# Optimization experiments

Measured on AMD Instinct MI355X. Metric: run time of the kernel, lower is better.

## Reference

```python
import jax, jax.numpy as jnp
import numpy as np

B, F, D = 16384, 32, 64
EPS = 1e-5


def layer_norm(x, g, b):
    m = x.mean(-1, keepdims=True)
    v = ((x - m) ** 2).mean(-1, keepdims=True)
    return (x - m) / jnp.sqrt(v + EPS) * g + b


def setup_inputs() -> dict:
    key = jax.random.key(0)
    ks = jax.random.split(key, 24)
    IN = F * D

    def w(k, shape, fan_in):
        return jax.random.normal(k, shape, dtype=jnp.float32) / np.sqrt(fan_in)

    return {
        "x": jax.random.normal(ks[0], (B, F, D), dtype=jnp.float32),
        # StaticGRN (mask branch): Linear(IN,D) -> ELU -> Linear(D,F); skip Linear(IN,F); GateAndNorm(F)
        "mw1": w(ks[1], (IN, D), IN), "mb1": jnp.zeros((D,), jnp.float32),
        "mw2": w(ks[2], (D, F), D), "mb2": jnp.zeros((F,), jnp.float32),
        "mlw": w(ks[3], (IN, F), IN), "mlb": jnp.zeros((F,), jnp.float32),
        "mgw": w(ks[4], (F, F), F), "mgb": jnp.zeros((F,), jnp.float32),
        "mlw2": w(ks[5], (F, F), F), "mlb2": jnp.zeros((F,), jnp.float32),
        "mgamma": jnp.ones((F,), jnp.float32), "mbeta": jnp.zeros((F,), jnp.float32),
        # Per-feature GRNNoContext params, stacked over F (batched small GEMMs)
        "w1": w(ks[6], (F, D, D), D), "b1": jnp.zeros((F, D), jnp.float32),
        "w2": w(ks[7], (F, D, D), D), "b2": jnp.zeros((F, D), jnp.float32),
        "gw": w(ks[8], (F, D, D), D), "gb": jnp.zeros((F, D), jnp.float32),
        "lw": w(ks[9], (F, D, D), D), "lb": jnp.zeros((F, D), jnp.float32),
        "gamma": jnp.ones((F, D), jnp.float32), "beta": jnp.zeros((F, D), jnp.float32),
    }


def reference(x, mw1, mb1, mw2, mb2, mlw, mlb, mgw, mgb, mlw2, mlb2, mgamma, mbeta,
              w1, b1, w2, b2, gw, gb, lw, lb, gamma, beta):
    b, f, d = x.shape
    flat = x.reshape(b, f * d)
    # StaticGRN mask branch (dropout is 0.0 -> identity)
    h = jax.nn.elu(flat @ mw1 + mb1) @ mw2 + mb2          # [B,F]
    res = flat @ mlw + mlb                                 # [B,F] skip path
    pre = jax.nn.sigmoid(h @ mgw + mgb) * (h @ mlw2 + mlb2) + res
    mask = jax.nn.softmax(layer_norm(pre, mgamma, mbeta), axis=-1)[:, None, :]  # [B,1,F]
    # Per-feature GRNs, batched over the feature axis
    hh = jax.nn.elu(jnp.einsum('bfd,fde->bfe', x, w1) + b1)
    hh = jnp.einsum('bfd,fde->bfe', hh, w2) + b2
    gate = jax.nn.sigmoid(jnp.einsum('bfd,fde->bfe', hh, gw) + gb)
    lin = jnp.einsum('bfd,fde->bfe', hh, lw) + lb
    vecs = layer_norm(gate * lin + x, gamma, beta)         # [B,F,D]
    out = jnp.einsum('bof,bfd->bod', mask, vecs)[:, 0, :]  # [B,D]
    return out, mask
```

## Files before the change

### kernel.cpp

```cpp
#include <hip/hip_runtime.h>
#include <hip/hip_bf16.h>
#include <math.h>

#define NB 16384
#define NF 32
#define ND 64
#define NIN 2048

typedef __attribute__((ext_vector_type(8))) short fragA;
typedef __attribute__((ext_vector_type(4))) float fragC;

#define MFMA(a, b, c) __builtin_amdgcn_mfma_f32_16x16x32_bf16((a), (b), (c), 0, 0, 0)

__device__ __forceinline__ short f2bf(float f) {
    union { float f; unsigned u; } v; v.f = f;
    return (short)((v.u + 0x7fffu + ((v.u >> 16) & 1u)) >> 16);
}
__device__ __forceinline__ fragA cvt8(const float* p) {
    const float4 a = *(const float4*)p;
    const float4 b = *(const float4*)(p + 4);
    union { __hip_bfloat162 h[4]; fragA f; } u;
    u.h[0] = __float22bfloat162_rn(make_float2(a.x, a.y));
    u.h[1] = __float22bfloat162_rn(make_float2(a.z, a.w));
    u.h[2] = __float22bfloat162_rn(make_float2(b.x, b.y));
    u.h[3] = __float22bfloat162_rn(make_float2(b.z, b.w));
    return u.f;
}

__global__ __launch_bounds__(256) void prep_kernel(
    const float* __restrict__ w1, const float* __restrict__ w2,
    const float* __restrict__ gw, const float* __restrict__ lw,
    const float* __restrict__ mw1, const float* __restrict__ mlw,
    const float* __restrict__ mw2, const float* __restrict__ mgw,
    const float* __restrict__ mlw2,
    short* __restrict__ wsout)
{
    int F = blockIdx.x * 256 + threadIdx.x;
    fragA o;
    if (F < 65536) {
        int mat = F >> 14;
        int f   = (F >> 9) & 31;
        int nt  = (F >> 7) & 3;
        int s   = (F >> 6) & 1;
        int l   = F & 63;
        const float* src = (mat == 0 ? w1 : mat == 1 ? w2 : mat == 2 ? gw : lw)
                           + (size_t)f * 4096;
        int n  = nt * 16 + (l & 15);
        int k0 = s * 32 + ((l >> 4) << 3);
#pragma unroll
        for (int j = 0; j < 8; ++j) o[j] = f2bf(src[(k0 + j) * 64 + n]);
    } else if (F < 90112) {
        int G  = F - 65536;
        int f  = G / 768;
        int r  = G - f * 768;
        int nt = r >> 7;
        int s  = (r >> 6) & 1;
        int l  = r & 63;
        int n  = nt * 16 + (l & 15);
        int k0 = f * 64 + s * 32 + ((l >> 4) << 3);
        if (n < 64) {
#pragma unroll
            for (int j = 0; j < 8; ++j) o[j] = f2bf(mw1[(size_t)(k0 + j) * 64 + n]);
        } else {
#pragma unroll
            for (int j = 0; j < 8; ++j) o[j] = f2bf(mlw[(size_t)(k0 + j) * 32 + (n - 64)]);
        }
    } else {
        int G2 = F - 90112;
        if (G2 < 256) {
            int nt = G2 >> 7, s = (G2 >> 6) & 1, l = G2 & 63;
            int n = nt * 16 + (l & 15);
            int k0 = s * 32 + ((l >> 4) << 3);
#pragma unroll
            for (int j = 0; j < 8; ++j) o[j] = f2bf(mw2[(k0 + j) * 32 + n]);
        } else {
            int G3 = G2 - 256;
            const float* src = (G3 < 128) ? mgw : mlw2;
            G3 &= 127;
            int nt = G3 >> 6, l = G3 & 63;
            int n = nt * 16 + (l & 15);
            int k0 = (l >> 4) << 3;
#pragma unroll
            for (int j = 0; j < 8; ++j) o[j] = f2bf(src[(k0 + j) * 32 + n]);
        }
    }
    ((fragA*)wsout)[F] = o;
}

__global__ __launch_bounds__(256, 4) void fused_kernel(
    const float* __restrict__ x,
    const short* __restrict__ wfrag, const short* __restrict__ mwfrag,
    const short* __restrict__ swfrag,
    const float* __restrict__ mb1, const float* __restrict__ mb2,
    const float* __restrict__ mlb, const float* __restrict__ mgb,
    const float* __restrict__ mlb2,
    const float* __restrict__ mgamma, const float* __restrict__ mbeta,
    const float* __restrict__ b1, const float* __restrict__ b2,
    const float* __restrict__ gb, const float* __restrict__ lb,
    const float* __restrict__ gamma, const float* __restrict__ beta,
    float* __restrict__ mask_out, float* __restrict__ out)
{
    __shared__ float smem[8960];
    float* redS  = smem;
    float* gS    = smem;
    float* lS    = smem + 768;
    float* hS1   = smem + 1552;
    float* resS  = smem + 2640;
    float* h2S   = smem + 3216;
    float* outS  = smem + 4352;
    float* maskS = smem + 8448;

    const int tid = threadIdx.x;
    const int w = tid >> 6, l = tid & 63;
    const int row0 = blockIdx.x * 16;
    const int m = l & 15, q = l >> 4;

    const fragA* wf  = (const fragA*)wfrag;
    const fragA* mwf = (const fragA*)mwfrag;
    const fragA* swf = (const fragA*)swfrag;

    for (int i = tid; i < 1552; i += 256) redS[i] = 0.f;
    __syncthreads();

    fragC acc[6];
#pragma unroll
    for (int nt = 0; nt < 6; ++nt) acc[nt] = (fragC){0.f, 0.f, 0.f, 0.f};

    const float* xpm = x + (size_t)(row0 + m) * NIN + q * 8;
    for (int fi = 0; fi < 8; ++fi) {
        int f = w * 8 + fi;
        const float* xp = xpm + f * ND;
        fragA a0 = cvt8(xp), a1 = cvt8(xp + 32);
        const size_t fb = (size_t)f * 768 + l;
#pragma unroll
        for (int nt = 0; nt < 6; ++nt) {
            acc[nt] = MFMA(a0, mwf[fb + nt * 128], acc[nt]);
            acc[nt] = MFMA(a1, mwf[fb + nt * 128 + 64], acc[nt]);
        }
    }
#pragma unroll
    for (int nt = 0; nt < 6; ++nt)
#pragma unroll
        for (int rg = 0; rg < 4; ++rg)
            atomicAdd(&redS[(q * 4 + rg) * 97 + nt * 16 + m], acc[nt][rg]);
    __syncthreads();

    {
        int r = tid & 15, cb = tid >> 4;
#pragma unroll
        for (int i = 0; i < 6; ++i) {
            int c = cb + i * 16;
            float s = redS[r * 97 + c];
            if (c < 64) {
                float v = s + mb1[c];
                hS1[r * 68 + c] = v > 0.f ? v : expm1f(v);
            } else {
                resS[r * 36 + (c - 64)] = s + mlb[c - 64];
            }
        }
    }
    __syncthreads();

    if (w < 2) {
        const float* ap = hS1 + m * 68 + q * 8;
        fragA a0 = cvt8(ap), a1 = cvt8(ap + 32);
        fragC c = {0.f, 0.f, 0.f, 0.f};
        c = MFMA(a0, swf[w * 128 + l], c);
        c = MFMA(a1, swf[w * 128 + 64 + l], c);
        float bv = mb2[w * 16 + m];
#pragma unroll
        for (int rg = 0; rg < 4; ++rg)
            h2S[(q * 4 + rg) * 36 + w * 16 + m] = c[rg] + bv;
    }
    __syncthreads();

    {
        int ntc = w & 1;
        int isl = w >> 1;
        fragA a = cvt8(h2S + m * 36 + q * 8);
        fragC c = {0.f, 0.f, 0.f, 0.f};
        c = MFMA(a, swf[256 + isl * 128 + ntc * 64 + l], c);
        float* dst = isl ? lS : gS;
#pragma unroll
        for (int rg = 0; rg < 4; ++rg)
            dst[(q * 4 + rg) * 36 + ntc * 16 + m] = c[rg];
    }
    __syncthreads();

    if (w == 0) {
        int r2 = l >> 2, c0 = (l & 3) * 8;
        float pre[8];
#pragma unroll
        for (int i = 0; i < 8; ++i) {
            int c = c0 + i;
            float gg = gS[r2 * 36 + c] + mgb[c];
            float ll = lS[r2 * 36 + c] + mlb2[c];
            pre[i] = ll / (1.f + expf(-gg)) + resS[r2 * 36 + c];
        }
        float s1 = 0.f;
#pragma unroll
        for (int i = 0; i < 8; ++i) s1 += pre[i];
        s1 += __shfl_xor(s1, 1); s1 += __shfl_xor(s1, 2);
        float mean = s1 * (1.f / 32.f);
        float s2 = 0.f;
#pragma unroll
        for (int i = 0; i < 8; ++i) { float d = pre[i] - mean; s2 += d * d; }
        s2 += __shfl_xor(s2, 1); s2 += __shfl_xor(s2, 2);
        float inv = rsqrtf(s2 * (1.f / 32.f) + 1e-5f);
        float ln[8]; float mx = -3.4e38f;
#pragma unroll
        for (int i = 0; i < 8; ++i) {
            ln[i] = (pre[i] - mean) * inv * mgamma[c0 + i] + mbeta[c0 + i];
            mx = fmaxf(mx, ln[i]);
        }
        mx = fmaxf(mx, __shfl_xor(mx, 1));
        mx = fmaxf(mx, __shfl_xor(mx, 2));
        float ssum = 0.f;
#pragma unroll
        for (int i = 0; i < 8; ++i) { ln[i] = expf(ln[i] - mx); ssum += ln[i]; }
        ssum += __shfl_xor(ssum, 1); ssum += __shfl_xor(ssum, 2);
        float rs = 1.f / ssum;
        float* mo = mask_out + (size_t)(row0 + r2) * 32 + c0;
        *(float4*)mo       = (float4){ln[0] * rs, ln[1] * rs, ln[2] * rs, ln[3] * rs};
        *(float4*)(mo + 4) = (float4){ln[4] * rs, ln[5] * rs, ln[6] * rs, ln[7] * rs};
#pragma unroll
        for (int i = 0; i < 8; ++i) maskS[r2 * 32 + c0 + i] = ln[i] * rs;
    }
    __syncthreads();

    float* hW = smem + w * 1088;

    fragC oac[4];
#pragma unroll
    for (int nt = 0; nt < 4; ++nt) oac[nt] = (fragC){0.f, 0.f, 0.f, 0.f};

    for (int fi = 0; fi < 8; ++fi) {
        int f = w * 8 + fi;
        float xres[4][4];
#pragma unroll
        for (int rg = 0; rg < 4; ++rg)
#pragma unroll
            for (int nt = 0; nt < 4; ++nt)
                xres[rg][nt] = x[(size_t)(row0 + q * 4 + rg) * NIN + f * ND + nt * 16 + m];
        float b1v[4], b2v[4], gbv[4], lbv[4], gmv[4], btv[4];
#pragma unroll
        for (int nt = 0; nt < 4; ++nt) {
            int c = f * 64 + nt * 16 + m;
            b1v[nt] = b1[c]; b2v[nt] = b2[c]; gbv[nt] = gb[c];
            lbv[nt] = lb[c]; gmv[nt] = gamma[c]; btv[nt] = beta[c];
        }
        float mk[4];
#pragma unroll
        for (int rg = 0; rg < 4; ++rg) mk[rg] = maskS[(q * 4 + rg) * 32 + f];

        {
            const float* xp = xpm + f * ND;
            fragA a0 = cvt8(xp), a1 = cvt8(xp + 32);
            const size_t base = (size_t)f * 512 + l;
#pragma unroll
            for (int nt = 0; nt < 4; ++nt) {
                fragC c = {0.f, 0.f, 0.f, 0.f};
                c = MFMA(a0, wf[base + nt * 128], c);
                c = MFMA(a1, wf[base + nt * 128 + 64], c);
                int col = nt * 16 + m;
#pragma unroll
                for (int rg = 0; rg < 4; ++rg) {
                    float v = c[rg] + b1v[nt];
                    hW[(q * 4 + rg) * 68 + col] = v > 0.f ? v : expm1f(v);
                }
            }
        }
        {
            const float* ap = hW + m * 68 + q * 8;
            fragA a0 = cvt8(ap), a1 = cvt8(ap + 32);
            const size_t base = ((size_t)(NF + f)) * 512 + l;
            fragC cc[4];
#pragma unroll
            for (int nt = 0; nt < 4; ++nt) {
                fragC c = {0.f, 0.f, 0.f, 0.f};
                c = MFMA(a0, wf[base + nt * 128], c);
                c = MFMA(a1, wf[base + nt * 128 + 64], c);
                cc[nt] = c;
            }
#pragma unroll
            for (int nt = 0; nt < 4; ++nt) {
                int col = nt * 16 + m;
#pragma unroll
                for (int rg = 0; rg < 4; ++rg)
                    hW[(q * 4 + rg) * 68 + col] = cc[nt][rg] + b2v[nt];
            }
        }
        {
            const float* ap = hW + m * 68 + q * 8;
            fragA a0 = cvt8(ap), a1 = cvt8(ap + 32);
            const size_t baseg = ((size_t)(2 * NF + f)) * 512 + l;
            const size_t basel = ((size_t)(3 * NF + f)) * 512 + l;
            fragC ga[4], la[4];
#pragma unroll
            for (int nt = 0; nt < 4; ++nt) {
                fragC g = {0.f, 0.f, 0.f, 0.f}, li = {0.f, 0.f, 0.f, 0.f};
                g  = MFMA(a0, wf[baseg + nt * 128], g);
                g  = MFMA(a1, wf[baseg + nt * 128 + 64], g);
                li = MFMA(a0, wf[basel + nt * 128], li);
                li = MFMA(a1, wf[basel + nt * 128 + 64], li);
                ga[nt] = g; la[nt] = li;
            }
#pragma unroll
            for (int rg = 0; rg < 4; ++rg) {
                float val[4];
#pragma unroll
                for (int nt = 0; nt < 4; ++nt) {
                    float gg = ga[nt][rg] + gbv[nt];
                    float ll = la[nt][rg] + lbv[nt];
                    val[nt] = ll / (1.f + expf(-gg)) + xres[rg][nt];
                }
                float s1 = val[0] + val[1] + val[2] + val[3];
                s1 += __shfl_xor(s1, 1); s1 += __shfl_xor(s1, 2);
                s1 += __shfl_xor(s1, 4); s1 += __shfl_xor(s1, 8);
                float mean = s1 * (1.f / 64.f);
                float s2 = 0.f;
#pragma unroll
                for (int nt = 0; nt < 4; ++nt) { float d = val[nt] - mean; s2 += d * d; }
                s2 += __shfl_xor(s2, 1); s2 += __shfl_xor(s2, 2);
                s2 += __shfl_xor(s2, 4); s2 += __shfl_xor(s2, 8);
                float inv = rsqrtf(s2 * (1.f / 64.f) + 1e-5f);
#pragma unroll
                for (int nt = 0; nt < 4; ++nt) {
                    float vec = (val[nt] - mean) * inv * gmv[nt] + btv[nt];
                    oac[nt][rg] += mk[rg] * vec;
                }
            }
        }
    }

#pragma unroll
    for (int nt = 0; nt < 4; ++nt)
#pragma unroll
        for (int rg = 0; rg < 4; ++rg)
            outS[w * 1024 + (q * 4 + rg) * 64 + nt * 16 + m] = oac[nt][rg];
    __syncthreads();
    {
        int t4 = tid * 4;
        int r = t4 >> 6, c = t4 & 63;
        float v[4];
#pragma unroll
        for (int j = 0; j < 4; ++j) {
            v[j] = outS[r * 64 + c + j] + outS[1024 + r * 64 + c + j]
                 + outS[2048 + r * 64 + c + j] + outS[3072 + r * 64 + c + j];
        }
        *(float4*)(out + (size_t)(row0 + r) * 64 + c) = (float4){v[0], v[1], v[2], v[3]};
    }
}

extern "C" void kernel_launch(void* const* d_in, const int* in_sizes, int n_in,
                              void* d_out, int out_size, void* d_ws, size_t ws_size,
                              hipStream_t stream) {
    const float* x      = (const float*)d_in[0];
    const float* mw1    = (const float*)d_in[1];
    const float* mb1    = (const float*)d_in[2];
    const float* mw2    = (const float*)d_in[3];
    const float* mb2    = (const float*)d_in[4];
    const float* mlw    = (const float*)d_in[5];
    const float* mlb    = (const float*)d_in[6];
    const float* mgw    = (const float*)d_in[7];
    const float* mgb    = (const float*)d_in[8];
    const float* mlw2   = (const float*)d_in[9];
    const float* mlb2   = (const float*)d_in[10];
    const float* mgamma = (const float*)d_in[11];
    const float* mbeta  = (const float*)d_in[12];
    const float* w1     = (const float*)d_in[13];
    const float* b1     = (const float*)d_in[14];
    const float* w2     = (const float*)d_in[15];
    const float* b2     = (const float*)d_in[16];
    const float* gw     = (const float*)d_in[17];
    const float* gb     = (const float*)d_in[18];
    const float* lw     = (const float*)d_in[19];
    const float* lb     = (const float*)d_in[20];
    const float* gamma  = (const float*)d_in[21];
    const float* beta   = (const float*)d_in[22];

    float* out  = (float*)d_out;
    float* mask = out + (size_t)NB * 64;

    short* wfrag  = (short*)d_ws;
    short* mwfrag = wfrag + (size_t)65536 * 8;
    short* swfrag = wfrag + (size_t)90112 * 8;

    hipLaunchKernelGGL(prep_kernel, dim3(354), dim3(256), 0, stream,
                       w1, w2, gw, lw, mw1, mlw, mw2, mgw, mlw2, wfrag);
    hipLaunchKernelGGL(fused_kernel, dim3(NB / 16), dim3(256), 0, stream,
                       x, wfrag, mwfrag, swfrag,
                       mb1, mb2, mlb, mgb, mlb2, mgamma, mbeta,
                       b1, b2, gb, lb, gamma, beta,
                       mask, out);
}
```

Measured before the change: 347.5 us.

## Replace LDS atomics with per-wave partials, fast-math epilogues, reorder per-feature GRN loads

The first-stage cross-wave reduction now has each wave write its partial tile to its own LDS slot, and one pass sums the four slots. This removes the zero-init pass, a barrier and the LDS atomics. ELU, sigmoid and softmax use __expf and hardware reciprocal, and layer norm computes sum and sum of squares in a single shuffle pass. The per-feature loop prefetches w2 fragments into registers and moves the residual, bias and mask loads to later points so their latency overlaps with MFMA work. Risks are lower accuracy from the fast intrinsics and the one-pass variance, plus higher register pressure from the prefetched fragments.

```diff
diff --git a/kernel.cpp b/kernel.cpp
--- a/kernel.cpp
+++ b/kernel.cpp
@@ -26,6 +26,10 @@
     u.h[3] = __float22bfloat162_rn(make_float2(b.z, b.w));
     return u.f;
 }
+
+__device__ __forceinline__ float frcp(float x) { return __builtin_amdgcn_rcpf(x); }
+__device__ __forceinline__ float felu(float v) { return v > 0.f ? v : __expf(v) - 1.f; }
+__device__ __forceinline__ float fsig(float g) { return __builtin_amdgcn_rcpf(1.f + __expf(-g)); }
 
 __global__ __launch_bounds__(256) void prep_kernel(
     const float* __restrict__ w1, const float* __restrict__ w2,
@@ -104,9 +108,9 @@
     float* redS  = smem;
     float* gS    = smem;
     float* lS    = smem + 768;
-    float* hS1   = smem + 1552;
-    float* resS  = smem + 2640;
-    float* h2S   = smem + 3216;
+    float* hS1   = smem + 6208;
+    float* resS  = smem + 7296;
+    float* h2S   = smem + 7872;
     float* outS  = smem + 4352;
     float* maskS = smem + 8448;
 
@@ -118,9 +122,6 @@
     const fragA* wf  = (const fragA*)wfrag;
     const fragA* mwf = (const fragA*)mwfrag;
     const fragA* swf = (const fragA*)swfrag;
-
-    for (int i = tid; i < 1552; i += 256) redS[i] = 0.f;
-    __syncthreads();
 
     fragC acc[6];
 #pragma unroll
@@ -138,11 +139,14 @@
             acc[nt] = MFMA(a1, mwf[fb + nt * 128 + 64], acc[nt]);
         }
     }
-#pragma unroll
-    for (int nt = 0; nt < 6; ++nt)
-#pragma unroll
-        for (int rg = 0; rg < 4; ++rg)
-            atomicAdd(&redS[(q * 4 + rg) * 97 + nt * 16 + m], acc[nt][rg]);
+    {
+        float* myred = redS + w * 1552;
+#pragma unroll
+        for (int nt = 0; nt < 6; ++nt)
+#pragma unroll
+            for (int rg = 0; rg < 4; ++rg)
+                myred[(q * 4 + rg) * 97 + nt * 16 + m] = acc[nt][rg];
+    }
     __syncthreads();
 
     {
@@ -150,10 +154,10 @@
 #pragma unroll
         for (int i = 0; i < 6; ++i) {
             int c = cb + i * 16;
-            float s = redS[r * 97 + c];
+            float s = redS[r * 97 + c]        + redS[1552 + r * 97 + c]
+                    + redS[3104 + r * 97 + c] + redS[4656 + r * 97 + c];
             if (c < 64) {
-                float v = s + mb1[c];
-                hS1[r * 68 + c] = v > 0.f ? v : expm1f(v);
+                hS1[r * 68 + c] = felu(s + mb1[c]);
             } else {
                 resS[r * 36 + (c - 64)] = s + mlb[c - 64];
             }
@@ -195,18 +199,16 @@
             int c = c0 + i;
             float gg = gS[r2 * 36 + c] + mgb[c];
             float ll = lS[r2 * 36 + c] + mlb2[c];
-            pre[i] = ll / (1.f + expf(-gg)) + resS[r2 * 36 + c];
-        }
-        float s1 = 0.f;
-#pragma unroll
-        for (int i = 0; i < 8; ++i) s1 += pre[i];
-        s1 += __shfl_xor(s1, 1); s1 += __shfl_xor(s1, 2);
+            pre[i] = ll * fsig(gg) + resS[r2 * 36 + c];
+        }
+        float s1 = 0.f, s2 = 0.f;
+#pragma unroll
+        for (int i = 0; i < 8; ++i) { s1 += pre[i]; s2 += pre[i] * pre[i]; }
+        s1 += __shfl_xor(s1, 1); s2 += __shfl_xor(s2, 1);
+        s1 += __shfl_xor(s1, 2); s2 += __shfl_xor(s2, 2);
         float mean = s1 * (1.f / 32.f);
-        float s2 = 0.f;
-#pragma unroll
-        for (int i = 0; i < 8; ++i) { float d = pre[i] - mean; s2 += d * d; }
-        s2 += __shfl_xor(s2, 1); s2 += __shfl_xor(s2, 2);
-        float inv = rsqrtf(s2 * (1.f / 32.f) + 1e-5f);
+        float var  = s2 * (1.f / 32.f) - mean * mean;
+        float inv  = rsqrtf(fmaxf(var, 0.f) + 1e-5f);
         float ln[8]; float mx = -3.4e38f;
 #pragma unroll
         for (int i = 0; i < 8; ++i) {
@@ -217,9 +219,9 @@
         mx = fmaxf(mx, __shfl_xor(mx, 2));
         float ssum = 0.f;
 #pragma unroll
-        for (int i = 0; i < 8; ++i) { ln[i] = expf(ln[i] - mx); ssum += ln[i]; }
+        for (int i = 0; i < 8; ++i) { ln[i] = __expf(ln[i] - mx); ssum += ln[i]; }
         ssum += __shfl_xor(ssum, 1); ssum += __shfl_xor(ssum, 2);
-        float rs = 1.f / ssum;
+        float rs = frcp(ssum);
         float* mo = mask_out + (size_t)(row0 + r2) * 32 + c0;
         *(float4*)mo       = (float4){ln[0] * rs, ln[1] * rs, ln[2] * rs, ln[3] * rs};
         *(float4*)(mo + 4) = (float4){ln[4] * rs, ln[5] * rs, ln[6] * rs, ln[7] * rs};
@@ -235,100 +237,105 @@
     for (int nt = 0; nt < 4; ++nt) oac[nt] = (fragC){0.f, 0.f, 0.f, 0.f};
 
     for (int fi = 0; fi < 8; ++fi) {
-        int f = w * 8 + fi;
+        const int f = w * 8 + fi;
+        const size_t base1 = (size_t)f * 512 + l;
+        const size_t base2 = (size_t)(NF + f) * 512 + l;
+        const size_t baseg = (size_t)(2 * NF + f) * 512 + l;
+        const size_t basel = (size_t)(3 * NF + f) * 512 + l;
+
+        const float* xp = xpm + f * ND;
+        fragA a0 = cvt8(xp), a1 = cvt8(xp + 32);
+        fragC c1[4];
+#pragma unroll
+        for (int nt = 0; nt < 4; ++nt) {
+            fragC c = {0.f, 0.f, 0.f, 0.f};
+            c = MFMA(a0, wf[base1 + nt * 128], c);
+            c = MFMA(a1, wf[base1 + nt * 128 + 64], c);
+            c1[nt] = c;
+        }
+        fragA w2f[8];
+#pragma unroll
+        for (int j = 0; j < 4; ++j) {
+            w2f[j]     = wf[base2 + j * 128];
+            w2f[j + 4] = wf[base2 + j * 128 + 64];
+        }
+#pragma unroll
+        for (int nt = 0; nt < 4; ++nt) {
+            float bv = b1[f * 64 + nt * 16 + m];
+            int col = nt * 16 + m;
+#pragma unroll
+            for (int rg = 0; rg < 4; ++rg)
+                hW[(q * 4 + rg) * 68 + col] = felu(c1[nt][rg] + bv);
+        }
+        const float* ap = hW + m * 68 + q * 8;
+        fragA h0 = cvt8(ap), h1 = cvt8(ap + 32);
+        fragC c2[4];
+#pragma unroll
+        for (int nt = 0; nt < 4; ++nt) {
+            fragC c = {0.f, 0.f, 0.f, 0.f};
+            c = MFMA(h0, w2f[nt], c);
+            c = MFMA(h1, w2f[nt + 4], c);
+            c2[nt] = c;
+        }
         float xres[4][4];
 #pragma unroll
         for (int rg = 0; rg < 4; ++rg)
 #pragma unroll
             for (int nt = 0; nt < 4; ++nt)
                 xres[rg][nt] = x[(size_t)(row0 + q * 4 + rg) * NIN + f * ND + nt * 16 + m];
-        float b1v[4], b2v[4], gbv[4], lbv[4], gmv[4], btv[4];
-#pragma unroll
-        for (int nt = 0; nt < 4; ++nt) {
-            int c = f * 64 + nt * 16 + m;
-            b1v[nt] = b1[c]; b2v[nt] = b2[c]; gbv[nt] = gb[c];
-            lbv[nt] = lb[c]; gmv[nt] = gamma[c]; btv[nt] = beta[c];
-        }
         float mk[4];
 #pragma unroll
         for (int rg = 0; rg < 4; ++rg) mk[rg] = maskS[(q * 4 + rg) * 32 + f];
-
-        {
-            const float* xp = xpm + f * ND;
-            fragA a0 = cvt8(xp), a1 = cvt8(xp + 32);
-            const size_t base = (size_t)f * 512 + l;
+#pragma unroll
+        for (int nt = 0; nt < 4; ++nt) {
+            float bv = b2[f * 64 + nt * 16 + m];
+            int col = nt * 16 + m;
+#pragma unroll
+            for (int rg = 0; rg < 4; ++rg)
+                hW[(q * 4 + rg) * 68 + col] = c2[nt][rg] + bv;
+        }
+        const float* ap2 = hW + m * 68 + q * 8;
+        fragA g0 = cvt8(ap2), g1 = cvt8(ap2 + 32);
+        fragC ga[4], la[4];
+#pragma unroll
+        for (int nt = 0; nt < 4; ++nt) {
+            fragC g = {0.f, 0.f, 0.f, 0.f}, li = {0.f, 0.f, 0.f, 0.f};
+            g  = MFMA(g0, wf[baseg + nt * 128], g);
+            g  = MFMA(g1, wf[baseg + nt * 128 + 64], g);
+            li = MFMA(g0, wf[basel + nt * 128], li);
+            li = MFMA(g1, wf[basel + nt * 128 + 64], li);
+            ga[nt] = g; la[nt] = li;
+        }
+        float gbv[4], lbv[4], gmv[4], btv[4];
+#pragma unroll
+        for (int nt = 0; nt < 4; ++nt) {
+            int cidx = f * 64 + nt * 16 + m;
+            gbv[nt] = gb[cidx]; lbv[nt] = lb[cidx];
+            gmv[nt] = gamma[cidx]; btv[nt] = beta[cidx];
+        }
+#pragma unroll
+        for (int rg = 0; rg < 4; ++rg) {
+            float val[4];
 #pragma unroll
             for (int nt = 0; nt < 4; ++nt) {
-                fragC c = {0.f, 0.f, 0.f, 0.f};
-                c = MFMA(a0, wf[base + nt * 128], c);
-                c = MFMA(a1, wf[base + nt * 128 + 64], c);
-                int col = nt * 16 + m;
-#pragma unroll
-                for (int rg = 0; rg < 4; ++rg) {
-                    float v = c[rg] + b1v[nt];
-                    hW[(q * 4 + rg) * 68 + col] = v > 0.f ? v : expm1f(v);
-                }
+                float gg = ga[nt][rg] + gbv[nt];
+                float ll = la[nt][rg] + lbv[nt];
+                val[nt] = ll * fsig(gg) + xres[rg][nt];
             }
-        }
-        {
-            const float* ap = hW + m * 68 + q * 8;
-            fragA a0 = cvt8(ap), a1 = cvt8(ap + 32);
-            const size_t base = ((size_t)(NF + f)) * 512 + l;
-            fragC cc[4];
+            float s1 = 0.f, s2 = 0.f;
+#pragma unroll
+            for (int nt = 0; nt < 4; ++nt) { s1 += val[nt]; s2 += val[nt] * val[nt]; }
+            s1 += __shfl_xor(s1, 1); s2 += __shfl_xor(s2, 1);
+            s1 += __shfl_xor(s1, 2); s2 += __shfl_xor(s2, 2);
+            s1 += __shfl_xor(s1, 4); s2 += __shfl_xor(s2, 4);
+            s1 += __shfl_xor(s1, 8); s2 += __shfl_xor(s2, 8);
+            float mean = s1 * (1.f / 64.f);
+            float var  = s2 * (1.f / 64.f) - mean * mean;
+            float inv  = rsqrtf(fmaxf(var, 0.f) + 1e-5f);
 #pragma unroll
             for (int nt = 0; nt < 4; ++nt) {
-                fragC c = {0.f, 0.f, 0.f, 0.f};
-                c = MFMA(a0, wf[base + nt * 128], c);
-                c = MFMA(a1, wf[base + nt * 128 + 64], c);
-                cc[nt] = c;
-            }
-#pragma unroll
-            for (int nt = 0; nt < 4; ++nt) {
-                int col = nt * 16 + m;
-#pragma unroll
-                for (int rg = 0; rg < 4; ++rg)
-                    hW[(q * 4 + rg) * 68 + col] = cc[nt][rg] + b2v[nt];
-            }
-        }
-        {
-            const float* ap = hW + m * 68 + q * 8;
-            fragA a0 = cvt8(ap), a1 = cvt8(ap + 32);
-            const size_t baseg = ((size_t)(2 * NF + f)) * 512 + l;
-            const size_t basel = ((size_t)(3 * NF + f)) * 512 + l;
-            fragC ga[4], la[4];
-#pragma unroll
-            for (int nt = 0; nt < 4; ++nt) {
-                fragC g = {0.f, 0.f, 0.f, 0.f}, li = {0.f, 0.f, 0.f, 0.f};
-                g  = MFMA(a0, wf[baseg + nt * 128], g);
-                g  = MFMA(a1, wf[baseg + nt * 128 + 64], g);
-                li = MFMA(a0, wf[basel + nt * 128], li);
-                li = MFMA(a1, wf[basel + nt * 128 + 64], li);
-                ga[nt] = g; la[nt] = li;
-            }
-#pragma unroll
-            for (int rg = 0; rg < 4; ++rg) {
-                float val[4];
-#pragma unroll
-                for (int nt = 0; nt < 4; ++nt) {
-                    float gg = ga[nt][rg] + gbv[nt];
-                    float ll = la[nt][rg] + lbv[nt];
-                    val[nt] = ll / (1.f + expf(-gg)) + xres[rg][nt];
-                }
-                float s1 = val[0] + val[1] + val[2] + val[3];
-                s1 += __shfl_xor(s1, 1); s1 += __shfl_xor(s1, 2);
-                s1 += __shfl_xor(s1, 4); s1 += __shfl_xor(s1, 8);
-                float mean = s1 * (1.f / 64.f);
-                float s2 = 0.f;
-#pragma unroll
-                for (int nt = 0; nt < 4; ++nt) { float d = val[nt] - mean; s2 += d * d; }
-                s2 += __shfl_xor(s2, 1); s2 += __shfl_xor(s2, 2);
-                s2 += __shfl_xor(s2, 4); s2 += __shfl_xor(s2, 8);
-                float inv = rsqrtf(s2 * (1.f / 64.f) + 1e-5f);
-#pragma unroll
-                for (int nt = 0; nt < 4; ++nt) {
-                    float vec = (val[nt] - mean) * inv * gmv[nt] + btv[nt];
-                    oac[nt][rg] += mk[rg] * vec;
-                }
+                float vec = (val[nt] - mean) * inv * gmv[nt] + btv[nt];
+                oac[nt][rg] += mk[rg] * vec;
             }
         }
     }
```

New measurement: 310.5 us. 10.7% less time.
